# Optimization experiments

Measured on AMD Instinct MI355X. Metric: run time of the kernel, lower is better.

## Reference

```python
import jax, jax.numpy as jnp
import numpy as np

HIDDEN = 1024
HEADS = 16
HEAD_DIM = HIDDEN // HEADS


def setup_inputs() -> dict:
    key = jax.random.key(0)
    ks = jax.random.split(key, 11)
    B, N, D = 2, 2048, HIDDEN
    scale = 1.0 / np.sqrt(D)
    inp = {
        "q": jax.random.normal(ks[0], (B, N, D), jnp.float32),
        "k": jax.random.normal(ks[1], (B, N, D), jnp.float32),
        "v": jax.random.normal(ks[2], (B, N, D), jnp.float32),
        "Wq": jax.random.normal(ks[3], (D, D), jnp.float32) * scale,
        "bq": jnp.zeros((D,), jnp.float32),
        "Wk": jax.random.normal(ks[4], (D, D), jnp.float32) * scale,
        "bk": jnp.zeros((D,), jnp.float32),
        "Wv": jax.random.normal(ks[5], (D, D), jnp.float32) * scale,
        "bv": jnp.zeros((D,), jnp.float32),
        "Wo": jax.random.normal(ks[6], (D, D), jnp.float32) * scale,
        "bo": jnp.zeros((D,), jnp.float32),
    }
    return inp


def _split_heads(x):  # [b, n, h*d] -> [b, h, n, d]
    b, n, _ = x.shape
    return x.reshape(b, n, HEADS, HEAD_DIM).transpose(0, 2, 1, 3)


def reference(q, k, v, Wq, bq, Wk, bk, Wv, bv, Wo, bo):
    # Linear projections (torch Linear: x @ W.T + b)
    Q = _split_heads(q @ Wq.T + bq)   # [b, h, n, d]
    K = _split_heads(k @ Wk.T + bk)   # [b, h, n, d]
    V = _split_heads(v @ Wv.T + bv)   # [b, h, n, d]
    scale = 1.0 / jnp.sqrt(jnp.asarray(HEAD_DIM, Q.dtype))
    scores = jnp.einsum("bhnd,bhmd->bhnm", Q, K) * scale  # [b, h, n, n]
    attn = jax.nn.softmax(scores, axis=-1)
    out = jnp.einsum("bhnm,bhmd->bhnd", attn, V)          # [b, h, n, d]
    b, h, n, d = out.shape
    out = out.transpose(0, 2, 1, 3).reshape(b, n, h * d)  # [b, n, h*d]
    return out @ Wo.T + bo
```

## Files before the change

### kernel.cpp

```cpp
#include <hip/hip_runtime.h>
#include <hip/hip_bf16.h>
#include <cstdint>
#include <cstddef>

#define DDIM 1024
#define NHEADS 16
#define HDIM 64
#define NSEQ 2048
#define NTOK 4096
#define QSCALE 0.18033688011112042f

typedef float f32x4 __attribute__((ext_vector_type(4)));
typedef float f32x16 __attribute__((ext_vector_type(16)));
typedef __bf16 bf16x8 __attribute__((ext_vector_type(8)));
typedef unsigned short u16x8 __attribute__((ext_vector_type(8)));

typedef __attribute__((address_space(1))) const unsigned int gq_t;
typedef __attribute__((address_space(3))) unsigned int lq_t;

__device__ __forceinline__ unsigned short f2bf(float f) {
    union { float f; unsigned int u; } v; v.f = f;
    unsigned int u = v.u;
    u += 0x7FFFu + ((u >> 16) & 1u);
    return (unsigned short)(u >> 16);
}

__device__ __forceinline__ float exp2_fast(float x) {
    float r;
    asm("v_exp_f32 %0, %1\n\ts_nop 0" : "=v"(r) : "v"(x));
    return r;
}

__device__ __forceinline__ unsigned cvtpk_bf16(float lo, float hi) {
    unsigned r;
    asm("v_cvt_pk_bf16_f32 %0, %1, %2" : "=v"(r) : "v"(lo), "v"(hi));
    return r;
}

#define PSWAP(a, b) asm("v_permlane32_swap_b32 %0, %1" : "+v"(a), "+v"(b))

__global__ __launch_bounds__(256) void cvt3_kernel(
    const float* __restrict__ a0, const float* __restrict__ a1,
    const float* __restrict__ a2, unsigned short* __restrict__ d0,
    unsigned short* __restrict__ d1, unsigned short* __restrict__ d2) {
    int z = blockIdx.z;
    const float* s = z == 0 ? a0 : z == 1 ? a1 : a2;
    unsigned short* d = z == 0 ? d0 : z == 1 ? d1 : d2;
    int i = blockIdx.x * 256 + threadIdx.x;
    const float4* s4 = (const float4*)s + (size_t)i * 2;
    float4 a = s4[0], b = s4[1];
    unsigned short o[8] __attribute__((aligned(16)));
    o[0] = f2bf(a.x); o[1] = f2bf(a.y); o[2] = f2bf(a.z); o[3] = f2bf(a.w);
    o[4] = f2bf(b.x); o[5] = f2bf(b.y); o[6] = f2bf(b.z); o[7] = f2bf(b.w);
    *(u16x8*)(d + (size_t)i * 8) = *(const u16x8*)o;
}

__global__ __launch_bounds__(256) void cvt4_kernel(
    const float* __restrict__ a0, const float* __restrict__ a1,
    const float* __restrict__ a2, const float* __restrict__ a3,
    unsigned short* __restrict__ d0, unsigned short* __restrict__ d1,
    unsigned short* __restrict__ d2, unsigned short* __restrict__ d3) {
    int z = blockIdx.z;
    const float* s = z == 0 ? a0 : z == 1 ? a1 : z == 2 ? a2 : a3;
    unsigned short* d = z == 0 ? d0 : z == 1 ? d1 : z == 2 ? d2 : d3;
    int i = blockIdx.x * 256 + threadIdx.x;
    const float4* s4 = (const float4*)s + (size_t)i * 2;
    float4 a = s4[0], b = s4[1];
    unsigned short o[8] __attribute__((aligned(16)));
    o[0] = f2bf(a.x); o[1] = f2bf(a.y); o[2] = f2bf(a.z); o[3] = f2bf(a.w);
    o[4] = f2bf(b.x); o[5] = f2bf(b.y); o[6] = f2bf(b.z); o[7] = f2bf(b.w);
    *(u16x8*)(d + (size_t)i * 8) = *(const u16x8*)o;
}

__device__ __forceinline__ void gemm_body(const unsigned short* __restrict__ A,
                                          const unsigned short* __restrict__ W,
                                          const float* __restrict__ bias,
                                          int mode, void* __restrict__ Cout) {
    __shared__ __align__(16) unsigned short As[128 * 32];
    __shared__ __align__(16) unsigned short Bs[128 * 32];
    const int tid = threadIdx.x, lane = tid & 63, wid = tid >> 6;
    const int r = lane & 15, g = lane >> 4;
    const int mbase = blockIdx.y * 128;
    const int nbase = blockIdx.x * 128;
    const int wm = (wid >> 1) * 64, wn = (wid & 1) * 64;

    f32x4 zero = {0.f, 0.f, 0.f, 0.f};
    f32x4 acc[4][4];
#pragma unroll
    for (int mi = 0; mi < 4; ++mi)
#pragma unroll
        for (int ni = 0; ni < 4; ++ni) acc[mi][ni] = zero;

    for (int kt = 0; kt < 1024; kt += 32) {
        __syncthreads();
#pragma unroll
        for (int j = 0; j < 2; ++j) {
            int ub = wid * 64 + j * 256;
            int uu = ub + lane;
            const unsigned short* ga =
                A + (size_t)(mbase + (uu >> 2)) * 1024 + kt + (uu & 3) * 8;
            __builtin_amdgcn_global_load_lds((gq_t*)ga, (lq_t*)(As + ub * 8), 16, 0, 0);
            const unsigned short* gb =
                W + (size_t)(nbase + (uu >> 2)) * 1024 + kt + (uu & 3) * 8;
            __builtin_amdgcn_global_load_lds((gq_t*)gb, (lq_t*)(Bs + ub * 8), 16, 0, 0);
        }
        __syncthreads();
        bf16x8 af[4], bf[4];
#pragma unroll
        for (int mi = 0; mi < 4; ++mi)
            af[mi] = *(const bf16x8*)(As + (wm + mi * 16 + r) * 32 + g * 8);
#pragma unroll
        for (int ni = 0; ni < 4; ++ni)
            bf[ni] = *(const bf16x8*)(Bs + (wn + ni * 16 + r) * 32 + g * 8);
#pragma unroll
        for (int mi = 0; mi < 4; ++mi)
#pragma unroll
            for (int ni = 0; ni < 4; ++ni)
                acc[mi][ni] = __builtin_amdgcn_mfma_f32_16x16x32_bf16(
                    af[mi], bf[ni], acc[mi][ni], 0, 0, 0);
    }
#pragma unroll
    for (int mi = 0; mi < 4; ++mi) {
#pragma unroll
        for (int ni = 0; ni < 4; ++ni) {
            int c = nbase + wn + ni * 16 + r;
            float bv = bias[c];
#pragma unroll
            for (int rr = 0; rr < 4; ++rr) {
                int m = mbase + wm + mi * 16 + g * 4 + rr;
                float val = acc[mi][ni][rr] + bv;
                if (mode == 0) {
                    ((unsigned short*)Cout)[(size_t)m * 1024 + c] = f2bf(val * QSCALE);
                } else if (mode == 1) {
                    size_t addr = ((size_t)((m >> 11) * 16 + (c >> 6)) * 2048 +
                                   (size_t)(m & 2047)) * 64 + (c & 63);
                    ((unsigned short*)Cout)[addr] = f2bf(val);
                } else if (mode == 2) {
                    ((unsigned short*)Cout)[(size_t)m * 1024 + c] = f2bf(val);
                } else {
                    ((float*)Cout)[(size_t)m * 1024 + c] = val;
                }
            }
        }
    }
}

__global__ __launch_bounds__(256) void gemm_qkv_kernel(
    const unsigned short* __restrict__ qb, const unsigned short* __restrict__ kb,
    const unsigned short* __restrict__ vb, const unsigned short* __restrict__ Wq,
    const unsigned short* __restrict__ Wk, const unsigned short* __restrict__ Wv,
    const float* __restrict__ bq, const float* __restrict__ bk,
    const float* __restrict__ bv, unsigned short* __restrict__ Qp,
    unsigned short* __restrict__ Kp, unsigned short* __restrict__ Vp) {
    int z = blockIdx.z;
    const unsigned short* A = (z == 0) ? qb : (z == 1) ? kb : vb;
    const unsigned short* W = (z == 0) ? Wq : (z == 1) ? Wk : Wv;
    const float* bias = (z == 0) ? bq : (z == 1) ? bk : bv;
    unsigned short* C = (z == 0) ? Qp : (z == 1) ? Kp : Vp;
    gemm_body(A, W, bias, z, C);
}

__global__ __launch_bounds__(256) void gemm_out_kernel(
    const unsigned short* __restrict__ AO, const unsigned short* __restrict__ Wo,
    const float* __restrict__ bo, float* __restrict__ out) {
    gemm_body(AO, Wo, bo, 3, out);
}

__global__ __launch_bounds__(256) void vtrans_kernel(
    const unsigned short* __restrict__ Vp, unsigned short* __restrict__ Vt) {
    __shared__ __align__(16) unsigned short T[64 * 80];
    const int tid = threadIdx.x;
    const int n0 = blockIdx.x * 64, bh = blockIdx.y;
    const int b = bh >> 4, h = bh & 15;
    const unsigned short* src = Vp + (size_t)(b * NSEQ + n0) * DDIM + h * HDIM;
#pragma unroll
    for (int j = 0; j < 2; ++j) {
        int idx = j * 256 + tid;
        int n = idx >> 3, c = (idx & 7) * 8;
        u16x8 val = *(const u16x8*)(src + (size_t)n * DDIM + c);
        *(u16x8*)(&T[n * 80 + c]) = val;
    }
    __syncthreads();
    unsigned short* dst = Vt + (size_t)bh * HDIM * NSEQ + n0;
#pragma unroll
    for (int j = 0; j < 2; ++j) {
        int idx = j * 256 + tid;
        int d = idx >> 3, nn = (idx & 7) * 8, rot = idx & 7;
        unsigned short o[8] __attribute__((aligned(16)));
#pragma unroll
        for (int e0 = 0; e0 < 8; ++e0) {
            int e = (e0 + rot) & 7;
            o[e] = T[(nn + e) * 80 + d];
        }
        *(u16x8*)(dst + (size_t)d * NSEQ + nn) = *(const u16x8*)o;
    }
}

__global__ __launch_bounds__(256, 2) void attn_kernel(
    const unsigned short* __restrict__ Qp,
    const unsigned short* __restrict__ Kh,
    const unsigned short* __restrict__ Vt,
    unsigned short* __restrict__ AO) {
    __shared__ __align__(16) unsigned short Ks[2][4096];
    __shared__ __align__(16) unsigned short Vs[2][4096];

    const int tid = threadIdx.x, lane = tid & 63, wid = tid >> 6;
    const int q31 = lane & 31, hi = lane >> 5;

    int bid = blockIdx.x;
    int swz = (bid & 7) * 64 + (bid >> 3);
    const int bh = swz >> 4, b = bh >> 4, h = bh & 15;
    const int qbase = ((swz & 15) * 4 + wid) * 32;

    const unsigned short* Kt = Kh + (size_t)bh * (NSEQ * HDIM);
    const unsigned short* Vb = Vt + (size_t)bh * (HDIM * NSEQ);

    bf16x8 qf[4];
    {
        const unsigned short* qp =
            Qp + (size_t)(b * NSEQ + qbase + q31) * DDIM + h * HDIM + hi * 8;
#pragma unroll
        for (int t = 0; t < 4; ++t) qf[t] = *(const bf16x8*)(qp + t * 16);
    }

    const size_t koff0 = (size_t)q31 * HDIM + (wid & 3) * 16 + hi * 8;
    const size_t koff1 = koff0 + 32 * HDIM;
    const size_t voff0 =
        (size_t)q31 * NSEQ + ((wid >> 1) & 1) * 32 + (wid & 1) * 16 + hi * 8;
    const size_t voff1 = voff0 + (size_t)32 * NSEQ;
    const int lb0 = wid * 512, lb1 = wid * 512 + 2048;

    auto STAGE = [&](int buf, int kv0) {
        const unsigned short* kbase = Kt + (size_t)kv0 * HDIM;
        __builtin_amdgcn_global_load_lds((gq_t*)(kbase + koff0),
                                         (lq_t*)(&Ks[buf][lb0]), 16, 0, 0);
        __builtin_amdgcn_global_load_lds((gq_t*)(kbase + koff1),
                                         (lq_t*)(&Ks[buf][lb1]), 16, 0, 0);
        const unsigned short* vbase = Vb + kv0;
        __builtin_amdgcn_global_load_lds((gq_t*)(vbase + voff0),
                                         (lq_t*)(&Vs[buf][lb0]), 16, 0, 0);
        __builtin_amdgcn_global_load_lds((gq_t*)(vbase + voff1),
                                         (lq_t*)(&Vs[buf][lb1]), 16, 0, 0);
    };

    f32x16 oA0, oB0, oA1, oB1;
#pragma unroll
    for (int i = 0; i < 16; ++i) {
        oA0[i] = 0.f; oB0[i] = 0.f; oA1[i] = 0.f; oB1[i] = 0.f;
    }
    float m0 = -3.0e38f, l0 = 0.f, m1 = -3.0e38f, l1 = 0.f;

    union PB { unsigned u[4]; bf16x8 v; };

    auto QK = [&](int cur, int s) -> f32x16 {
        const unsigned short* kf = &Ks[cur][s * 2048 + lane * 8];
        f32x16 st;
#pragma unroll
        for (int i = 0; i < 16; ++i) st[i] = 0.f;
#pragma unroll
        for (int t = 0; t < 4; ++t)
            st = __builtin_amdgcn_mfma_f32_32x32x16_bf16(
                *(const bf16x8*)(kf + t * 512), qf[t], st, 0, 0, 0);
        return st;
    };

    auto SM = [&](const f32x16& st, float& m, float& l, f32x16& oA, f32x16& oB,
                  PB& P0, PB& P1) {
        float m8[8], m4[4];
#pragma unroll
        for (int j = 0; j < 8; ++j) m8[j] = fmaxf(st[2 * j], st[2 * j + 1]);
#pragma unroll
        for (int j = 0; j < 4; ++j) m4[j] = fmaxf(m8[2 * j], m8[2 * j + 1]);
        float pm = fmaxf(fmaxf(m4[0], m4[1]), fmaxf(m4[2], m4[3]));
        pm = fmaxf(pm, __shfl_xor(pm, 32, 64));

        if (__any(pm - m > 8.0f)) {
            float mn = fmaxf(m, pm);
            float al = exp2_fast(m - mn);
            m = mn;
            l *= al;
#pragma unroll
            for (int i = 0; i < 16; ++i) { oA[i] *= al; oB[i] *= al; }
        }

        float p[16];
#pragma unroll
        for (int i = 0; i < 16; ++i) p[i] = exp2_fast(st[i] - m);
        float s8[8], s4[4];
#pragma unroll
        for (int j = 0; j < 8; ++j) s8[j] = p[2 * j] + p[2 * j + 1];
#pragma unroll
        for (int j = 0; j < 4; ++j) s4[j] = s8[2 * j] + s8[2 * j + 1];
        float rs = (s4[0] + s4[1]) + (s4[2] + s4[3]);
        rs += __shfl_xor(rs, 32, 64);
        l += rs;

        unsigned w0 = cvtpk_bf16(p[0], p[1]), w1 = cvtpk_bf16(p[2], p[3]);
        unsigned w2 = cvtpk_bf16(p[4], p[5]), w3 = cvtpk_bf16(p[6], p[7]);
        unsigned w4 = cvtpk_bf16(p[8], p[9]), w5 = cvtpk_bf16(p[10], p[11]);
        unsigned w6 = cvtpk_bf16(p[12], p[13]), w7 = cvtpk_bf16(p[14], p[15]);
        PSWAP(w0, w2); PSWAP(w1, w3); PSWAP(w4, w6); PSWAP(w5, w7);
        P0.u[0] = w0; P0.u[1] = w1; P0.u[2] = w2; P0.u[3] = w3;
        P1.u[0] = w4; P1.u[1] = w5; P1.u[2] = w6; P1.u[3] = w7;
    };

    auto PV = [&](int cur, int s, const PB& P0, const PB& P1, f32x16& oA,
                  f32x16& oB) {
        const unsigned short* vf0 = &Vs[cur][s * 1024 + lane * 8];
        const unsigned short* vf1 = &Vs[cur][2048 + s * 1024 + lane * 8];
        oA = __builtin_amdgcn_mfma_f32_32x32x16_bf16(
            *(const bf16x8*)(vf0), P0.v, oA, 0, 0, 0);
        oA = __builtin_amdgcn_mfma_f32_32x32x16_bf16(
            *(const bf16x8*)(vf0 + 512), P1.v, oA, 0, 0, 0);
        oB = __builtin_amdgcn_mfma_f32_32x32x16_bf16(
            *(const bf16x8*)(vf1), P0.v, oB, 0, 0, 0);
        oB = __builtin_amdgcn_mfma_f32_32x32x16_bf16(
            *(const bf16x8*)(vf1 + 512), P1.v, oB, 0, 0, 0);
    };

    STAGE(0, 0);
    int cur = 0;
    for (int it = 0; it < 32; ++it) {
        STAGE(cur ^ 1, ((it + 1) & 31) * 64);
        asm volatile("s_waitcnt vmcnt(4)" ::: "memory");
        __builtin_amdgcn_s_barrier();
        __builtin_amdgcn_sched_barrier(0);
        __builtin_amdgcn_s_setprio(1);
        f32x16 st0 = QK(cur, 0);
        f32x16 st1 = QK(cur, 1);
        __builtin_amdgcn_s_setprio(0);
        PB P00, P01, P10, P11;
        SM(st0, m0, l0, oA0, oB0, P00, P01);
        SM(st1, m1, l1, oA1, oB1, P10, P11);
        __builtin_amdgcn_s_setprio(1);
        PV(cur, 0, P00, P01, oA0, oB0);
        PV(cur, 1, P10, P11, oA1, oB1);
        __builtin_amdgcn_s_setprio(0);
        __builtin_amdgcn_sched_barrier(0);
        asm volatile("" ::: "memory");
        __builtin_amdgcn_s_barrier();
        cur ^= 1;
    }

    float mt = fmaxf(m0, m1);
    float a0 = exp2_fast(m0 - mt), a1 = exp2_fast(m1 - mt);
    float inv = 1.0f / (l0 * a0 + l1 * a1);
    unsigned short* op = AO + (size_t)(b * NSEQ + qbase + q31) * DDIM + h * HDIM;
#pragma unroll
    for (int r2 = 0; r2 < 16; ++r2) {
        int d = (r2 & 3) + 8 * (r2 >> 2) + 4 * hi;
        op[d] = f2bf((oA0[r2] * a0 + oA1[r2] * a1) * inv);
        op[d + 32] = f2bf((oB0[r2] * a0 + oB1[r2] * a1) * inv);
    }
}

extern "C" void kernel_launch(void* const* d_in, const int* in_sizes, int n_in,
                              void* d_out, int out_size, void* d_ws, size_t ws_size,
                              hipStream_t stream) {
    const float* q = (const float*)d_in[0];
    const float* k = (const float*)d_in[1];
    const float* v = (const float*)d_in[2];
    const float* Wq = (const float*)d_in[3];
    const float* bq = (const float*)d_in[4];
    const float* Wk = (const float*)d_in[5];
    const float* bk = (const float*)d_in[6];
    const float* Wv = (const float*)d_in[7];
    const float* bv = (const float*)d_in[8];
    const float* Wo = (const float*)d_in[9];
    const float* bo = (const float*)d_in[10];
    float* out = (float*)d_out;

    unsigned short* ws = (unsigned short*)d_ws;
    const size_t TOKD = (size_t)NTOK * DDIM;
    const size_t WD = (size_t)DDIM * DDIM;
    unsigned short* qb = ws;
    unsigned short* kb = qb + TOKD;
    unsigned short* vb = kb + TOKD;
    unsigned short* Wqb = vb + TOKD;
    unsigned short* Wkb = Wqb + WD;
    unsigned short* Wvb = Wkb + WD;
    unsigned short* Wob = Wvb + WD;
    unsigned short* Qp = Wob + WD;
    unsigned short* Kp = Qp + TOKD;
    unsigned short* Vp = Kp + TOKD;
    unsigned short* AOp = Vp + TOKD;
    unsigned short* Vtb = qb;

    const int tok8 = (int)(TOKD / 8);
    const int w8 = (int)(WD / 8);
    cvt3_kernel<<<dim3(tok8 / 256, 1, 3), 256, 0, stream>>>(q, k, v, qb, kb, vb);
    cvt4_kernel<<<dim3(w8 / 256, 1, 4), 256, 0, stream>>>(Wq, Wk, Wv, Wo,
                                                          Wqb, Wkb, Wvb, Wob);
    gemm_qkv_kernel<<<dim3(8, 32, 3), 256, 0, stream>>>(qb, kb, vb, Wqb, Wkb, Wvb,
                                                        bq, bk, bv, Qp, Kp, Vp);
    vtrans_kernel<<<dim3(32, 32), 256, 0, stream>>>(Vp, Vtb);
    attn_kernel<<<512, 256, 0, stream>>>(Qp, Kp, Vtb, AOp);
    gemm_out_kernel<<<dim3(8, 32), 256, 0, stream>>>(AOp, Wob, bo, out);
}
```

Measured before the change: 149.9 us.

## Double-buffer GEMM LDS staging, reorder tile layout, fuse V transpose into epilogue

The GEMM main loop now double-buffers the A/B tiles in LDS, issuing the next tile's global-to-LDS loads before computing on the current one. It uses vmcnt waits and raw barriers in place of two __syncthreads per iteration, and raises wave priority around the MFMA block. The LDS tile layout changes so each lane's fragment reads are contiguous. The V projection epilogue writes directly in transposed head-major layout with packed 4-element stores, which removes the separate vtrans kernel and its extra pass over V. The cost is doubled LDS use per block, which may reduce occupancy.

```diff
diff --git a/kernel.cpp b/kernel.cpp
--- a/kernel.cpp
+++ b/kernel.cpp
@@ -76,14 +76,28 @@
                                           const unsigned short* __restrict__ W,
                                           const float* __restrict__ bias,
                                           int mode, void* __restrict__ Cout) {
-    __shared__ __align__(16) unsigned short As[128 * 32];
-    __shared__ __align__(16) unsigned short Bs[128 * 32];
+    __shared__ __align__(16) unsigned short As[2][4096];
+    __shared__ __align__(16) unsigned short Bs[2][4096];
     const int tid = threadIdx.x, lane = tid & 63, wid = tid >> 6;
     const int r = lane & 15, g = lane >> 4;
     const int mbase = blockIdx.y * 128;
     const int nbase = blockIdx.x * 128;
     const int wm = (wid >> 1) * 64, wn = (wid & 1) * 64;
 
+    const size_t sro = (size_t)(wid * 16 + (lane & 15)) * 1024 + (lane >> 4) * 8;
+
+    auto STAGE = [&](int buf, int kt) {
+#pragma unroll
+        for (int j = 0; j < 2; ++j) {
+            const unsigned short* ga = A + (size_t)(mbase + j * 64) * 1024 + kt + sro;
+            __builtin_amdgcn_global_load_lds(
+                (gq_t*)ga, (lq_t*)(&As[buf][(j * 256 + wid * 64) * 8]), 16, 0, 0);
+            const unsigned short* gb = W + (size_t)(nbase + j * 64) * 1024 + kt + sro;
+            __builtin_amdgcn_global_load_lds(
+                (gq_t*)gb, (lq_t*)(&Bs[buf][(j * 256 + wid * 64) * 8]), 16, 0, 0);
+        }
+    };
+
     f32x4 zero = {0.f, 0.f, 0.f, 0.f};
     f32x4 acc[4][4];
 #pragma unroll
@@ -91,55 +105,66 @@
 #pragma unroll
         for (int ni = 0; ni < 4; ++ni) acc[mi][ni] = zero;
 
-    for (int kt = 0; kt < 1024; kt += 32) {
-        __syncthreads();
-#pragma unroll
-        for (int j = 0; j < 2; ++j) {
-            int ub = wid * 64 + j * 256;
-            int uu = ub + lane;
-            const unsigned short* ga =
-                A + (size_t)(mbase + (uu >> 2)) * 1024 + kt + (uu & 3) * 8;
-            __builtin_amdgcn_global_load_lds((gq_t*)ga, (lq_t*)(As + ub * 8), 16, 0, 0);
-            const unsigned short* gb =
-                W + (size_t)(nbase + (uu >> 2)) * 1024 + kt + (uu & 3) * 8;
-            __builtin_amdgcn_global_load_lds((gq_t*)gb, (lq_t*)(Bs + ub * 8), 16, 0, 0);
-        }
-        __syncthreads();
+    STAGE(0, 0);
+    int cur = 0;
+    for (int it = 0; it < 32; ++it) {
+        STAGE(cur ^ 1, ((it + 1) & 31) * 32);
+        asm volatile("s_waitcnt vmcnt(4)" ::: "memory");
+        __builtin_amdgcn_s_barrier();
+        __builtin_amdgcn_sched_barrier(0);
+        const unsigned short* afp = &As[cur][(wid >> 1) * 2048 + lane * 8];
+        const unsigned short* bfp = &Bs[cur][(wid & 1) * 2048 + lane * 8];
         bf16x8 af[4], bf[4];
 #pragma unroll
-        for (int mi = 0; mi < 4; ++mi)
-            af[mi] = *(const bf16x8*)(As + (wm + mi * 16 + r) * 32 + g * 8);
-#pragma unroll
-        for (int ni = 0; ni < 4; ++ni)
-            bf[ni] = *(const bf16x8*)(Bs + (wn + ni * 16 + r) * 32 + g * 8);
+        for (int mi = 0; mi < 4; ++mi) af[mi] = *(const bf16x8*)(afp + mi * 512);
+#pragma unroll
+        for (int ni = 0; ni < 4; ++ni) bf[ni] = *(const bf16x8*)(bfp + ni * 512);
+        __builtin_amdgcn_s_setprio(1);
 #pragma unroll
         for (int mi = 0; mi < 4; ++mi)
 #pragma unroll
             for (int ni = 0; ni < 4; ++ni)
                 acc[mi][ni] = __builtin_amdgcn_mfma_f32_16x16x32_bf16(
                     af[mi], bf[ni], acc[mi][ni], 0, 0, 0);
-    }
+        __builtin_amdgcn_s_setprio(0);
+        __builtin_amdgcn_sched_barrier(0);
+        asm volatile("" ::: "memory");
+        __builtin_amdgcn_s_barrier();
+        cur ^= 1;
+    }
+
 #pragma unroll
     for (int mi = 0; mi < 4; ++mi) {
 #pragma unroll
         for (int ni = 0; ni < 4; ++ni) {
             int c = nbase + wn + ni * 16 + r;
             float bv = bias[c];
-#pragma unroll
-            for (int rr = 0; rr < 4; ++rr) {
-                int m = mbase + wm + mi * 16 + g * 4 + rr;
-                float val = acc[mi][ni][rr] + bv;
-                if (mode == 0) {
-                    ((unsigned short*)Cout)[(size_t)m * 1024 + c] = f2bf(val * QSCALE);
-                } else if (mode == 1) {
-                    size_t addr = ((size_t)((m >> 11) * 16 + (c >> 6)) * 2048 +
-                                   (size_t)(m & 2047)) * 64 + (c & 63);
-                    ((unsigned short*)Cout)[addr] = f2bf(val);
-                } else if (mode == 2) {
-                    ((unsigned short*)Cout)[(size_t)m * 1024 + c] = f2bf(val);
-                } else {
-                    ((float*)Cout)[(size_t)m * 1024 + c] = val;
-                }
+            float v4[4];
+#pragma unroll
+            for (int rr = 0; rr < 4; ++rr) v4[rr] = acc[mi][ni][rr] + bv;
+            int m0 = mbase + wm + mi * 16 + g * 4;
+            if (mode == 0) {
+#pragma unroll
+                for (int rr = 0; rr < 4; ++rr)
+                    ((unsigned short*)Cout)[(size_t)(m0 + rr) * 1024 + c] =
+                        f2bf(v4[rr] * QSCALE);
+            } else if (mode == 1) {
+                size_t base = ((size_t)((m0 >> 11) * 16 + (c >> 6)) * 2048 +
+                               (size_t)(m0 & 2047)) * 64 + (c & 63);
+#pragma unroll
+                for (int rr = 0; rr < 4; ++rr)
+                    ((unsigned short*)Cout)[base + (size_t)rr * 64] = f2bf(v4[rr]);
+            } else if (mode == 2) {
+                unsigned short o4[4] __attribute__((aligned(8)));
+#pragma unroll
+                for (int rr = 0; rr < 4; ++rr) o4[rr] = f2bf(v4[rr]);
+                size_t base = ((size_t)((m0 >> 11) * 16 + (c >> 6)) * 64 +
+                               (c & 63)) * 2048 + (size_t)(m0 & 2047);
+                *(ushort4*)((unsigned short*)Cout + base) = *(const ushort4*)o4;
+            } else {
+#pragma unroll
+                for (int rr = 0; rr < 4; ++rr)
+                    ((float*)Cout)[(size_t)(m0 + rr) * 1024 + c] = v4[rr];
             }
         }
     }
@@ -164,36 +189,6 @@
     const unsigned short* __restrict__ AO, const unsigned short* __restrict__ Wo,
     const float* __restrict__ bo, float* __restrict__ out) {
     gemm_body(AO, Wo, bo, 3, out);
-}
-
-__global__ __launch_bounds__(256) void vtrans_kernel(
-    const unsigned short* __restrict__ Vp, unsigned short* __restrict__ Vt) {
-    __shared__ __align__(16) unsigned short T[64 * 80];
-    const int tid = threadIdx.x;
-    const int n0 = blockIdx.x * 64, bh = blockIdx.y;
-    const int b = bh >> 4, h = bh & 15;
-    const unsigned short* src = Vp + (size_t)(b * NSEQ + n0) * DDIM + h * HDIM;
-#pragma unroll
-    for (int j = 0; j < 2; ++j) {
-        int idx = j * 256 + tid;
-        int n = idx >> 3, c = (idx & 7) * 8;
-        u16x8 val = *(const u16x8*)(src + (size_t)n * DDIM + c);
-        *(u16x8*)(&T[n * 80 + c]) = val;
-    }
-    __syncthreads();
-    unsigned short* dst = Vt + (size_t)bh * HDIM * NSEQ + n0;
-#pragma unroll
-    for (int j = 0; j < 2; ++j) {
-        int idx = j * 256 + tid;
-        int d = idx >> 3, nn = (idx & 7) * 8, rot = idx & 7;
-        unsigned short o[8] __attribute__((aligned(16)));
-#pragma unroll
-        for (int e0 = 0; e0 < 8; ++e0) {
-            int e = (e0 + rot) & 7;
-            o[e] = T[(nn + e) * 80 + d];
-        }
-        *(u16x8*)(dst + (size_t)d * NSEQ + nn) = *(const u16x8*)o;
-    }
 }
 
 __global__ __launch_bounds__(256, 2) void attn_kernel(
@@ -384,7 +379,6 @@
     unsigned short* Kp = Qp + TOKD;
     unsigned short* Vp = Kp + TOKD;
     unsigned short* AOp = Vp + TOKD;
-    unsigned short* Vtb = qb;
 
     const int tok8 = (int)(TOKD / 8);
     const int w8 = (int)(WD / 8);
@@ -393,7 +387,6 @@
                                                           Wqb, Wkb, Wvb, Wob);
     gemm_qkv_kernel<<<dim3(8, 32, 3), 256, 0, stream>>>(qb, kb, vb, Wqb, Wkb, Wvb,
                                                         bq, bk, bv, Qp, Kp, Vp);
-    vtrans_kernel<<<dim3(32, 32), 256, 0, stream>>>(Vp, Vtb);
-    attn_kernel<<<512, 256, 0, stream>>>(Qp, Kp, Vtb, AOp);
+    attn_kernel<<<512, 256, 0, stream>>>(Qp, Kp, Vp, AOp);
     gemm_out_kernel<<<dim3(8, 32), 256, 0, stream>>>(AOp, Wob, bo, out);
 }
```

New measurement: 165.5 us. 10.4% more time.

## Split attention KV range in two with a combine pass; merge convert kernels

Applied to the files above, without the earlier changes.

The attention kernel now splits each head's key/value sequence into two halves, launching 1024 blocks instead of 512. Each block writes a normalized partial output plus per-row max and sum, and a new combine kernel merges the two halves with log-sum-exp weights. The three-input and four-weight conversion kernels are also merged into one launch. The aim is to fill the GPU better during attention and drop a launch, at the cost of extra global traffic, an extra kernel, and a second bf16 rounding of partial outputs.

```diff
diff --git a/kernel.cpp b/kernel.cpp
--- a/kernel.cpp
+++ b/kernel.cpp
@@ -25,6 +25,12 @@
     return (unsigned short)(u >> 16);
 }
 
+__device__ __forceinline__ float bf2f(unsigned short s) {
+    union { unsigned int u; float f; } v;
+    v.u = (unsigned int)s << 16;
+    return v.f;
+}
+
 __device__ __forceinline__ float exp2_fast(float x) {
     float r;
     asm("v_exp_f32 %0, %1\n\ts_nop 0" : "=v"(r) : "v"(x));
@@ -39,31 +45,23 @@
 
 #define PSWAP(a, b) asm("v_permlane32_swap_b32 %0, %1" : "+v"(a), "+v"(b))
 
-__global__ __launch_bounds__(256) void cvt3_kernel(
-    const float* __restrict__ a0, const float* __restrict__ a1,
-    const float* __restrict__ a2, unsigned short* __restrict__ d0,
-    unsigned short* __restrict__ d1, unsigned short* __restrict__ d2) {
-    int z = blockIdx.z;
-    const float* s = z == 0 ? a0 : z == 1 ? a1 : a2;
-    unsigned short* d = z == 0 ? d0 : z == 1 ? d1 : d2;
-    int i = blockIdx.x * 256 + threadIdx.x;
-    const float4* s4 = (const float4*)s + (size_t)i * 2;
-    float4 a = s4[0], b = s4[1];
-    unsigned short o[8] __attribute__((aligned(16)));
-    o[0] = f2bf(a.x); o[1] = f2bf(a.y); o[2] = f2bf(a.z); o[3] = f2bf(a.w);
-    o[4] = f2bf(b.x); o[5] = f2bf(b.y); o[6] = f2bf(b.z); o[7] = f2bf(b.w);
-    *(u16x8*)(d + (size_t)i * 8) = *(const u16x8*)o;
-}
-
-__global__ __launch_bounds__(256) void cvt4_kernel(
+__global__ __launch_bounds__(256) void cvt_all_kernel(
     const float* __restrict__ a0, const float* __restrict__ a1,
     const float* __restrict__ a2, const float* __restrict__ a3,
-    unsigned short* __restrict__ d0, unsigned short* __restrict__ d1,
-    unsigned short* __restrict__ d2, unsigned short* __restrict__ d3) {
+    const float* __restrict__ a4, const float* __restrict__ a5,
+    const float* __restrict__ a6, unsigned short* __restrict__ d0,
+    unsigned short* __restrict__ d1, unsigned short* __restrict__ d2,
+    unsigned short* __restrict__ d3, unsigned short* __restrict__ d4,
+    unsigned short* __restrict__ d5, unsigned short* __restrict__ d6,
+    int tok8, int w8) {
     int z = blockIdx.z;
-    const float* s = z == 0 ? a0 : z == 1 ? a1 : z == 2 ? a2 : a3;
-    unsigned short* d = z == 0 ? d0 : z == 1 ? d1 : z == 2 ? d2 : d3;
+    const float* s = z == 0 ? a0 : z == 1 ? a1 : z == 2 ? a2 : z == 3 ? a3
+                     : z == 4 ? a4 : z == 5 ? a5 : a6;
+    unsigned short* d = z == 0 ? d0 : z == 1 ? d1 : z == 2 ? d2 : z == 3 ? d3
+                        : z == 4 ? d4 : z == 5 ? d5 : d6;
+    int n8 = (z < 3) ? tok8 : w8;
     int i = blockIdx.x * 256 + threadIdx.x;
+    if (i >= n8) return;
     const float4* s4 = (const float4*)s + (size_t)i * 2;
     float4 a = s4[0], b = s4[1];
     unsigned short o[8] __attribute__((aligned(16)));
@@ -200,7 +198,8 @@
     const unsigned short* __restrict__ Qp,
     const unsigned short* __restrict__ Kh,
     const unsigned short* __restrict__ Vt,
-    unsigned short* __restrict__ AO) {
+    unsigned short* __restrict__ AOs,
+    float2* __restrict__ ML) {
     __shared__ __align__(16) unsigned short Ks[2][4096];
     __shared__ __align__(16) unsigned short Vs[2][4096];
 
@@ -208,9 +207,13 @@
     const int q31 = lane & 31, hi = lane >> 5;
 
     int bid = blockIdx.x;
-    int swz = (bid & 7) * 64 + (bid >> 3);
-    const int bh = swz >> 4, b = bh >> 4, h = bh & 15;
-    const int qbase = ((swz & 15) * 4 + wid) * 32;
+    const int xcd = bid & 7, j = bid >> 3;
+    const int bh = xcd * 4 + (j >> 5);
+    const int split = (j >> 4) & 1;
+    const int qt = j & 15;
+    const int b = bh >> 4, h = bh & 15;
+    const int qbase = qt * 128 + wid * 32;
+    const int kvbase = split * 1024;
 
     const unsigned short* Kt = Kh + (size_t)bh * (NSEQ * HDIM);
     const unsigned short* Vb = Vt + (size_t)bh * (HDIM * NSEQ);
@@ -268,9 +271,9 @@
                   PB& P0, PB& P1) {
         float m8[8], m4[4];
 #pragma unroll
-        for (int j = 0; j < 8; ++j) m8[j] = fmaxf(st[2 * j], st[2 * j + 1]);
-#pragma unroll
-        for (int j = 0; j < 4; ++j) m4[j] = fmaxf(m8[2 * j], m8[2 * j + 1]);
+        for (int j2 = 0; j2 < 8; ++j2) m8[j2] = fmaxf(st[2 * j2], st[2 * j2 + 1]);
+#pragma unroll
+        for (int j2 = 0; j2 < 4; ++j2) m4[j2] = fmaxf(m8[2 * j2], m8[2 * j2 + 1]);
         float pm = fmaxf(fmaxf(m4[0], m4[1]), fmaxf(m4[2], m4[3]));
         pm = fmaxf(pm, __shfl_xor(pm, 32, 64));
 
@@ -288,9 +291,9 @@
         for (int i = 0; i < 16; ++i) p[i] = exp2_fast(st[i] - m);
         float s8[8], s4[4];
 #pragma unroll
-        for (int j = 0; j < 8; ++j) s8[j] = p[2 * j] + p[2 * j + 1];
-#pragma unroll
-        for (int j = 0; j < 4; ++j) s4[j] = s8[2 * j] + s8[2 * j + 1];
+        for (int j2 = 0; j2 < 8; ++j2) s8[j2] = p[2 * j2] + p[2 * j2 + 1];
+#pragma unroll
+        for (int j2 = 0; j2 < 4; ++j2) s4[j2] = s8[2 * j2] + s8[2 * j2 + 1];
         float rs = (s4[0] + s4[1]) + (s4[2] + s4[3]);
         rs += __shfl_xor(rs, 32, 64);
         l += rs;
@@ -318,10 +321,10 @@
             *(const bf16x8*)(vf1 + 512), P1.v, oB, 0, 0, 0);
     };
 
-    STAGE(0, 0);
+    STAGE(0, kvbase);
     int cur = 0;
-    for (int it = 0; it < 32; ++it) {
-        STAGE(cur ^ 1, ((it + 1) & 31) * 64);
+    for (int it = 0; it < 16; ++it) {
+        STAGE(cur ^ 1, kvbase + ((it + 1) & 15) * 64);
         asm volatile("s_waitcnt vmcnt(4)" ::: "memory");
         __builtin_amdgcn_s_barrier();
         __builtin_amdgcn_sched_barrier(0);
@@ -344,14 +347,47 @@
 
     float mt = fmaxf(m0, m1);
     float a0 = exp2_fast(m0 - mt), a1 = exp2_fast(m1 - mt);
-    float inv = 1.0f / (l0 * a0 + l1 * a1);
-    unsigned short* op = AO + (size_t)(b * NSEQ + qbase + q31) * DDIM + h * HDIM;
+    float l = l0 * a0 + l1 * a1;
+    float inv = 1.0f / l;
+    unsigned short* op = AOs + (size_t)split * ((size_t)NTOK * DDIM) +
+                         (size_t)(b * NSEQ + qbase + q31) * DDIM + h * HDIM;
 #pragma unroll
     for (int r2 = 0; r2 < 16; ++r2) {
         int d = (r2 & 3) + 8 * (r2 >> 2) + 4 * hi;
         op[d] = f2bf((oA0[r2] * a0 + oA1[r2] * a1) * inv);
         op[d + 32] = f2bf((oB0[r2] * a0 + oB1[r2] * a1) * inv);
     }
+    if (hi == 0) {
+        float2 ml; ml.x = mt; ml.y = l;
+        ML[((size_t)split * 32 + bh) * NSEQ + (qbase + q31)] = ml;
+    }
+}
+
+__global__ __launch_bounds__(256) void combine_kernel(
+    const unsigned short* __restrict__ O0, const unsigned short* __restrict__ O1,
+    const float2* __restrict__ ML, unsigned short* __restrict__ AO) {
+    int i = blockIdx.x * 256 + threadIdx.x;
+    int row = i >> 7;
+    int cg8 = (i & 127) * 8;
+    int h = cg8 >> 6;
+    int bh = (row >> 11) * 16 + h;
+    int q = row & 2047;
+    float2 ml0 = ML[(size_t)bh * NSEQ + q];
+    float2 ml1 = ML[((size_t)32 + bh) * NSEQ + q];
+    float M = fmaxf(ml0.x, ml1.x);
+    float w0 = ml0.y * exp2_fast(ml0.x - M);
+    float w1 = ml1.y * exp2_fast(ml1.x - M);
+    float inv = 1.0f / (w0 + w1);
+    w0 *= inv; w1 *= inv;
+    size_t off = (size_t)row * DDIM + cg8;
+    u16x8 a = *(const u16x8*)(O0 + off);
+    u16x8 c = *(const u16x8*)(O1 + off);
+    unsigned short o[8] __attribute__((aligned(16)));
+#pragma unroll
+    for (int e = 0; e < 8; ++e)
+        o[e] = f2bf(w0 * bf2f((unsigned short)a[e]) +
+                    w1 * bf2f((unsigned short)c[e]));
+    *(u16x8*)(AO + off) = *(const u16x8*)o;
 }
 
 extern "C" void kernel_launch(void* const* d_in, const int* in_sizes, int n_in,
@@ -385,15 +421,17 @@
     unsigned short* Vp = Kp + TOKD;
     unsigned short* AOp = Vp + TOKD;
     unsigned short* Vtb = qb;
+    unsigned short* AOs = kb;
+    float2* ML = (float2*)Wqb;
 
     const int tok8 = (int)(TOKD / 8);
     const int w8 = (int)(WD / 8);
-    cvt3_kernel<<<dim3(tok8 / 256, 1, 3), 256, 0, stream>>>(q, k, v, qb, kb, vb);
-    cvt4_kernel<<<dim3(w8 / 256, 1, 4), 256, 0, stream>>>(Wq, Wk, Wv, Wo,
-                                                          Wqb, Wkb, Wvb, Wob);
+    cvt_all_kernel<<<dim3(tok8 / 256, 1, 7), 256, 0, stream>>>(
+        q, k, v, Wq, Wk, Wv, Wo, qb, kb, vb, Wqb, Wkb, Wvb, Wob, tok8, w8);
     gemm_qkv_kernel<<<dim3(8, 32, 3), 256, 0, stream>>>(qb, kb, vb, Wqb, Wkb, Wvb,
                                                         bq, bk, bv, Qp, Kp, Vp);
     vtrans_kernel<<<dim3(32, 32), 256, 0, stream>>>(Vp, Vtb);
-    attn_kernel<<<512, 256, 0, stream>>>(Qp, Kp, Vtb, AOp);
+    attn_kernel<<<1024, 256, 0, stream>>>(Qp, Kp, Vtb, AOs, ML);
+    combine_kernel<<<2048, 256, 0, stream>>>(AOs, AOs + TOKD, ML, AOp);
     gemm_out_kernel<<<dim3(8, 32), 256, 0, stream>>>(AOp, Wob, bo, out);
 }
```

Result: slower. 162.1 us (+8.1%).
